# Performance work log

Hardware: AMD Instinct MI355X
Metric: run time of the kernel (lower is better)

Reference implementation:

```python
import jax, jax.numpy as jnp
import numpy as np

EMBED = 1024
HIDDEN = 1024

def setup_inputs() -> dict:
    key = jax.random.key(0)
    k1, k2, k3, k4, k5 = jax.random.split(key, 5)
    B, T = 32, 512
    s_ih = 1.0 / np.sqrt(HIDDEN)
    x = jax.random.normal(k1, (B, T, EMBED), dtype=jnp.float32)
    # PyTorch nn.RNN params: W_ih [H,E], W_hh [H,H], b_ih [H], b_hh [H], init U(-1/sqrt(H), 1/sqrt(H))
    W_ih = jax.random.uniform(k2, (HIDDEN, EMBED), minval=-s_ih, maxval=s_ih, dtype=jnp.float32)
    W_hh = jax.random.uniform(k3, (HIDDEN, HIDDEN), minval=-s_ih, maxval=s_ih, dtype=jnp.float32)
    b_ih = jax.random.uniform(k4, (HIDDEN,), minval=-s_ih, maxval=s_ih, dtype=jnp.float32)
    b_hh = jax.random.uniform(k5, (HIDDEN,), minval=-s_ih, maxval=s_ih, dtype=jnp.float32)
    return {"x": x, "W_ih": W_ih, "W_hh": W_hh, "b_ih": b_ih, "b_hh": b_hh}

def reference(x, W_ih, W_hh, b_ih, b_hh):
    # h_t = tanh(x_t @ W_ih^T + b_ih + h_{t-1} @ W_hh^T + b_hh), h_0 = 0
    B, T, E = x.shape
    H = W_hh.shape[0]
    # Precompute the input projection for all timesteps in one big GEMM.
    xp = jnp.einsum('bte,he->bth', x, W_ih) + (b_ih + b_hh)  # [B,T,H]
    h0 = jnp.zeros((B, H), dtype=x.dtype)

    def step(h, xp_t):
        h_new = jnp.tanh(xp_t + h @ W_hh.T)
        return h_new, h_new

    _, outs = jax.lax.scan(step, h0, jnp.swapaxes(xp, 0, 1))  # outs: [T,B,H]
    return jnp.swapaxes(outs, 0, 1)  # [B,T,H]
```

## Files before the change

kernel.cpp:

```cpp
#include <hip/hip_runtime.h>
#include <stdint.h>

#define B_ 32
#define T_ 512
#define E_ 1024
#define H_ 1024
#define NWAVE 64

typedef __attribute__((ext_vector_type(8))) short short8;
typedef __attribute__((ext_vector_type(4))) float floatx4;
typedef __attribute__((ext_vector_type(4))) int int4v;
typedef unsigned long long ull;

union U16 { ull u[2]; short8 s; int4v v; };

__device__ __forceinline__ unsigned short bf16_of(float f) {
    unsigned u = __float_as_uint(f);
    return (unsigned short)((u + 0x8000u) >> 16);
}

__device__ __forceinline__ short8 load_bf8(const float* __restrict__ p) {
    const float4* q = (const float4*)p;
    float4 v0 = q[0];
    float4 v1 = q[1];
    short8 r;
    r[0] = (short)bf16_of(v0.x); r[1] = (short)bf16_of(v0.y);
    r[2] = (short)bf16_of(v0.z); r[3] = (short)bf16_of(v0.w);
    r[4] = (short)bf16_of(v1.x); r[5] = (short)bf16_of(v1.y);
    r[6] = (short)bf16_of(v1.z); r[7] = (short)bf16_of(v1.w);
    return r;
}

__global__ __launch_bounds__(256) void k_xp(const float* __restrict__ x,
                                            const float* __restrict__ Wih,
                                            const float* __restrict__ bih,
                                            const float* __restrict__ bhh,
                                            float* __restrict__ out) {
    const int tid  = threadIdx.x;
    const int w    = tid >> 6;
    const int lane = tid & 63;
    const int l15  = lane & 15;
    const int quad = lane >> 4;
    const int rb = blockIdx.x >> 3;
    const int cb = blockIdx.x & 7;
    const int row_base = rb * 128 + w * 32;
    const int col_base = cb * 128;

    floatx4 acc[2][8];
#pragma unroll
    for (int i = 0; i < 2; i++)
#pragma unroll
        for (int j = 0; j < 8; j++) acc[i][j] = (floatx4)0.0f;

    for (int k0 = 0; k0 < E_; k0 += 32) {
        const int koff = k0 + quad * 8;
        short8 a[2];
#pragma unroll
        for (int mt = 0; mt < 2; mt++)
            a[mt] = load_bf8(x + (size_t)(row_base + mt * 16 + l15) * E_ + koff);
        short8 b[8];
#pragma unroll
        for (int nt = 0; nt < 8; nt++)
            b[nt] = load_bf8(Wih + (size_t)(col_base + nt * 16 + l15) * E_ + koff);
#pragma unroll
        for (int mt = 0; mt < 2; mt++)
#pragma unroll
            for (int nt = 0; nt < 8; nt++)
                acc[mt][nt] = __builtin_amdgcn_mfma_f32_16x16x32_bf16(
                    a[mt], b[nt], acc[mt][nt], 0, 0, 0);
    }

#pragma unroll
    for (int nt = 0; nt < 8; nt++) {
        const int col = col_base + nt * 16 + l15;
        const float bias = bih[col] + bhh[col];
#pragma unroll
        for (int mt = 0; mt < 2; mt++) {
            const int row = row_base + mt * 16 + quad * 4;
#pragma unroll
            for (int r = 0; r < 4; r++)
                out[(size_t)(row + r) * H_ + col] = acc[mt][nt][r] + bias;
        }
    }
}

__global__ void k_init(unsigned* __restrict__ ws, int ring) {
    const int i = blockIdx.x * blockDim.x + threadIdx.x;
    if (i < 1024) ws[i] = 0u;
    ws[1024 + (ring - 1) * 16384 + i] = 0u;
}

__global__ __launch_bounds__(128, 1) void k_rnn(const float* __restrict__ Whh,
                                                float* __restrict__ out,
                                                unsigned* __restrict__ ws,
                                                int ring) {
    const int tid  = threadIdx.x;
    const int wv   = tid >> 6;
    const int lane = tid & 63;
    const int wid  = blockIdx.x;
    const int j0   = wid * 16;

    unsigned* flags = ws;

    __shared__ unsigned short sh_h[512];
    __shared__ float sh_hf[2][512];
    __shared__ float sh_xp[2][512];

    if (wv == 0) {
        const int l15  = lane & 15;
        const int quad = lane >> 4;
        const int mt_s = lane >> 5;
        const int sub  = (lane >> 4) & 1;
        const int m_s  = lane & 15;
        const int slot = (wid >> 1) * 128 + mt_s * 64 + (wid & 1) * 32 + sub * 16 + m_s;
        const int lds_off = mt_s * 512 + m_s * 32 + sub * 16;

        short8 wreg[32];
#pragma unroll
        for (int c = 0; c < 32; c++)
            wreg[c] = load_bf8(Whh + (size_t)(j0 + l15) * H_ + c * 32 + quad * 8);

        __syncthreads();

#pragma unroll 1
        for (int t = 0; t < T_; t++) {
            const int rs  = (t + ring - 1) & (ring - 1);
            const int wsl = t & (ring - 1);
            const ull* hA = (const ull*)(ws + 1024 + rs * 16384);
            const ull* hB = hA + 4096;
            ull* nxA = (ull*)(ws + 1024 + wsl * 16384);
            ull* nxB = nxA + 4096;

            if (t > 0) {
                const unsigned tv = (unsigned)t;
                while (true) {
                    unsigned v = __hip_atomic_load(&flags[lane * 16],
                                                   __ATOMIC_RELAXED,
                                                   __HIP_MEMORY_SCOPE_AGENT);
                    if (__ballot(v < tv) == 0ull) break;
                }
                if ((t & (ring - 1)) == 0)
                    __builtin_amdgcn_fence(__ATOMIC_ACQUIRE, "agent");
                else
                    asm volatile("" ::: "memory");
            }

            floatx4 acc[2];
            acc[0] = (floatx4)0.0f;
            acc[1] = (floatx4)0.0f;
#pragma unroll
            for (int c = 0; c < 32; c++) {
#pragma unroll
                for (int mt = 0; mt < 2; mt++) {
                    U16 u;
                    u.u[0] = hA[(c * 2 + mt) * 64 + lane];
                    u.u[1] = hB[(c * 2 + mt) * 64 + lane];
                    acc[mt] = __builtin_amdgcn_mfma_f32_16x16x32_bf16(
                        u.s, wreg[c], acc[mt], 0, 0, 0);
                }
            }

#pragma unroll
            for (int mt = 0; mt < 2; mt++)
#pragma unroll
                for (int r = 0; r < 4; r++) {
                    const int b = mt * 16 + quad * 4 + r;
                    const float p = sh_xp[t & 1][b * 16 + l15] + acc[mt][r];
                    const float h = 1.0f - 2.0f / (__expf(2.0f * p) + 1.0f);
                    sh_hf[t & 1][b * 16 + l15] = h;
                    sh_h[b * 16 + l15] = bf16_of(h);
                }

            U16 pk;
            pk.v = *(const int4v*)((const char*)sh_h + lds_off);
            __hip_atomic_store(nxA + slot, pk.u[0], __ATOMIC_RELAXED,
                               __HIP_MEMORY_SCOPE_AGENT);
            __hip_atomic_store(nxB + slot, pk.u[1], __ATOMIC_RELAXED,
                               __HIP_MEMORY_SCOPE_AGENT);

            asm volatile("s_waitcnt vmcnt(0)" ::: "memory");
            if (lane == 0)
                __hip_atomic_store(&flags[wid * 16], (unsigned)(t + 1),
                                   __ATOMIC_RELAXED, __HIP_MEMORY_SCOPE_AGENT);

            __syncthreads();
        }
    } else {
        const int b  = lane >> 1;
        const int cs = (lane & 1) * 8;
        const float* xp_base = out + (size_t)b * T_ * H_ + j0 + cs;
        float*       out_base = out + (size_t)b * T_ * H_ + j0 + cs;

        {
            float4 v0 = *(const float4*)(xp_base + 0);
            float4 v1 = *(const float4*)(xp_base + 4);
            *(float4*)&sh_xp[0][b * 16 + cs]     = v0;
            *(float4*)&sh_xp[0][b * 16 + cs + 4] = v1;
        }
        __syncthreads();

        float hold[8];
#pragma unroll 1
        for (int t = 0; t < T_; t++) {
            float4 v0, v1;
            const bool more = (t + 1 < T_);
            if (more) {
                v0 = *(const float4*)(xp_base + (size_t)(t + 1) * H_);
                v1 = *(const float4*)(xp_base + (size_t)(t + 1) * H_ + 4);
            }
            if (t > 0) {
#pragma unroll
                for (int k = 0; k < 8; k++)
                    __builtin_nontemporal_store(
                        hold[k], out_base + (size_t)(t - 1) * H_ + k);
            }
            if (more) {
                *(float4*)&sh_xp[(t + 1) & 1][b * 16 + cs]     = v0;
                *(float4*)&sh_xp[(t + 1) & 1][b * 16 + cs + 4] = v1;
            }
            __syncthreads();
#pragma unroll
            for (int k = 0; k < 8; k++)
                hold[k] = sh_hf[t & 1][b * 16 + cs + k];
        }
#pragma unroll
        for (int k = 0; k < 8; k++)
            __builtin_nontemporal_store(hold[k],
                                        out_base + (size_t)(T_ - 1) * H_ + k);
    }
}

extern "C" void kernel_launch(void* const* d_in, const int* in_sizes, int n_in,
                              void* d_out, int out_size, void* d_ws, size_t ws_size,
                              hipStream_t stream) {
    const float* x   = (const float*)d_in[0];
    const float* Wih = (const float*)d_in[1];
    const float* Whh = (const float*)d_in[2];
    const float* bih = (const float*)d_in[3];
    const float* bhh = (const float*)d_in[4];
    float* out = (float*)d_out;
    unsigned* ws = (unsigned*)d_ws;

    const size_t need8 = (size_t)(1024 + 8 * 16384) * sizeof(unsigned);
    const int ring = (ws_size >= need8) ? 8 : 2;

    k_init<<<64, 256, 0, stream>>>(ws, ring);
    k_xp<<<128 * 8, 256, 0, stream>>>(x, Wih, bih, bhh, out);
    k_rnn<<<NWAVE, 128, 0, stream>>>(Whh, out, ws, ring);
}
```

Baseline: 2.584 ms.

## Pack four compute waves per block to cut grid-wide flag polling to sixteen

Instead of 64 single-compute-wave blocks, the recurrent kernel now runs 16 blocks, each holding four MFMA waves plus two store/prefetch waves. Each block joins its four waves with a __syncthreads and publishes one flag, so the per-step poll reads only 16 flags instead of 64. This shrinks cross-block synchronization cost per timestep. In exchange, every step adds an intra-block barrier before the flag store, and only 16 CUs carry the work. The helper waves also switch to wider 16-float vector loads and stores.

Result: slower. 9.043 ms (+249.9%).

```diff
diff --git a/kernel.cpp b/kernel.cpp
--- a/kernel.cpp
+++ b/kernel.cpp
@@ -5,7 +5,7 @@
 #define T_ 512
 #define E_ 1024
 #define H_ 1024
-#define NWAVE 64
+#define NBLK 16
 
 typedef __attribute__((ext_vector_type(8))) short short8;
 typedef __attribute__((ext_vector_type(4))) float floatx4;
@@ -90,30 +90,31 @@
     ws[1024 + (ring - 1) * 16384 + i] = 0u;
 }
 
-__global__ __launch_bounds__(128, 1) void k_rnn(const float* __restrict__ Whh,
+__global__ __launch_bounds__(384, 1) void k_rnn(const float* __restrict__ Whh,
                                                 float* __restrict__ out,
                                                 unsigned* __restrict__ ws,
                                                 int ring) {
     const int tid  = threadIdx.x;
     const int wv   = tid >> 6;
     const int lane = tid & 63;
-    const int wid  = blockIdx.x;
-    const int j0   = wid * 16;
+    const int bid  = blockIdx.x;
 
     unsigned* flags = ws;
 
-    __shared__ unsigned short sh_h[512];
-    __shared__ float sh_hf[2][512];
-    __shared__ float sh_xp[2][512];
-
-    if (wv == 0) {
+    __shared__ unsigned short sh_h[4 * 512];
+    __shared__ float sh_hf[2][2048];
+    __shared__ float sh_xp[2][2048];
+
+    if (wv < 4) {
+        const int wid  = bid * 4 + wv;
+        const int j0   = wid * 16;
         const int l15  = lane & 15;
         const int quad = lane >> 4;
         const int mt_s = lane >> 5;
         const int sub  = (lane >> 4) & 1;
         const int m_s  = lane & 15;
         const int slot = (wid >> 1) * 128 + mt_s * 64 + (wid & 1) * 32 + sub * 16 + m_s;
-        const int lds_off = mt_s * 512 + m_s * 32 + sub * 16;
+        const int lds_off = wv * 1024 + mt_s * 512 + m_s * 32 + sub * 16;
 
         short8 wreg[32];
 #pragma unroll
@@ -134,7 +135,7 @@
             if (t > 0) {
                 const unsigned tv = (unsigned)t;
                 while (true) {
-                    unsigned v = __hip_atomic_load(&flags[lane * 16],
+                    unsigned v = __hip_atomic_load(&flags[(lane & 15) * 16],
                                                    __ATOMIC_RELAXED,
                                                    __HIP_MEMORY_SCOPE_AGENT);
                     if (__ballot(v < tv) == 0ull) break;
@@ -165,10 +166,10 @@
 #pragma unroll
                 for (int r = 0; r < 4; r++) {
                     const int b = mt * 16 + quad * 4 + r;
-                    const float p = sh_xp[t & 1][b * 16 + l15] + acc[mt][r];
+                    const float p = sh_xp[t & 1][b * 64 + wv * 16 + l15] + acc[mt][r];
                     const float h = 1.0f - 2.0f / (__expf(2.0f * p) + 1.0f);
-                    sh_hf[t & 1][b * 16 + l15] = h;
-                    sh_h[b * 16 + l15] = bf16_of(h);
+                    sh_hf[t & 1][b * 64 + wv * 16 + l15] = h;
+                    sh_h[wv * 512 + b * 16 + l15] = bf16_of(h);
                 }
 
             U16 pk;
@@ -179,54 +180,56 @@
                                __HIP_MEMORY_SCOPE_AGENT);
 
             asm volatile("s_waitcnt vmcnt(0)" ::: "memory");
-            if (lane == 0)
-                __hip_atomic_store(&flags[wid * 16], (unsigned)(t + 1),
+
+            __syncthreads();
+
+            if (wv == 0 && lane == 0)
+                __hip_atomic_store(&flags[bid * 16], (unsigned)(t + 1),
                                    __ATOMIC_RELAXED, __HIP_MEMORY_SCOPE_AGENT);
-
-            __syncthreads();
         }
     } else {
-        const int b  = lane >> 1;
-        const int cs = (lane & 1) * 8;
-        const float* xp_base = out + (size_t)b * T_ * H_ + j0 + cs;
-        float*       out_base = out + (size_t)b * T_ * H_ + j0 + cs;
-
-        {
-            float4 v0 = *(const float4*)(xp_base + 0);
-            float4 v1 = *(const float4*)(xp_base + 4);
-            *(float4*)&sh_xp[0][b * 16 + cs]     = v0;
-            *(float4*)&sh_xp[0][b * 16 + cs + 4] = v1;
-        }
+        const int svl = tid - 256;
+        const int b   = svl >> 2;
+        const int cs  = (svl & 3) * 16;
+        const float* xp_base  = out + (size_t)b * T_ * H_ + bid * 64 + cs;
+        float*       out_base = out + (size_t)b * T_ * H_ + bid * 64 + cs;
+
+#pragma unroll
+        for (int k = 0; k < 4; k++)
+            *(floatx4*)&sh_xp[0][b * 64 + cs + 4 * k] =
+                *(const floatx4*)(xp_base + 4 * k);
         __syncthreads();
 
-        float hold[8];
+        floatx4 hold[4];
 #pragma unroll 1
         for (int t = 0; t < T_; t++) {
-            float4 v0, v1;
+            floatx4 v[4];
             const bool more = (t + 1 < T_);
             if (more) {
-                v0 = *(const float4*)(xp_base + (size_t)(t + 1) * H_);
-                v1 = *(const float4*)(xp_base + (size_t)(t + 1) * H_ + 4);
+#pragma unroll
+                for (int k = 0; k < 4; k++)
+                    v[k] = *(const floatx4*)(xp_base + (size_t)(t + 1) * H_ + 4 * k);
             }
             if (t > 0) {
 #pragma unroll
-                for (int k = 0; k < 8; k++)
+                for (int k = 0; k < 4; k++)
                     __builtin_nontemporal_store(
-                        hold[k], out_base + (size_t)(t - 1) * H_ + k);
+                        hold[k], (floatx4*)(out_base + (size_t)(t - 1) * H_ + 4 * k));
             }
             if (more) {
-                *(float4*)&sh_xp[(t + 1) & 1][b * 16 + cs]     = v0;
-                *(float4*)&sh_xp[(t + 1) & 1][b * 16 + cs + 4] = v1;
+#pragma unroll
+                for (int k = 0; k < 4; k++)
+                    *(floatx4*)&sh_xp[(t + 1) & 1][b * 64 + cs + 4 * k] = v[k];
             }
             __syncthreads();
 #pragma unroll
-            for (int k = 0; k < 8; k++)
-                hold[k] = sh_hf[t & 1][b * 16 + cs + k];
+            for (int k = 0; k < 4; k++)
+                hold[k] = *(const floatx4*)&sh_hf[t & 1][b * 64 + cs + 4 * k];
         }
 #pragma unroll
-        for (int k = 0; k < 8; k++)
-            __builtin_nontemporal_store(hold[k],
-                                        out_base + (size_t)(T_ - 1) * H_ + k);
+        for (int k = 0; k < 4; k++)
+            __builtin_nontemporal_store(
+                hold[k], (floatx4*)(out_base + (size_t)(T_ - 1) * H_ + 4 * k));
     }
 }
 
@@ -246,5 +249,5 @@
 
     k_init<<<64, 256, 0, stream>>>(ws, ring);
     k_xp<<<128 * 8, 256, 0, stream>>>(x, Wih, bih, bhh, out);
-    k_rnn<<<NWAVE, 128, 0, stream>>>(Whh, out, ws, ring);
-}
+    k_rnn<<<NBLK, 384, 0, stream>>>(Whh, out, ws, ring);
+}
```
